# Kernel tuning notes

Measured on AMD Instinct MI355X. Metric: run time of the kernel, lower is better.

The kernel has to match this reference:

```python
import jax, jax.numpy as jnp
import numpy as np

N, F, E, A, H = 50000, 64, 1600000, 8, 16
RECEPTIVE_FIELD = 7


def setup_inputs() -> dict:
    key = jax.random.key(0)
    ks = jax.random.split(key, 12)
    inp = {
        "x": jax.random.normal(ks[0], (N, F), dtype=jnp.float32),
        "edge_index": jax.random.randint(ks[1], (2, E), 0, N, dtype=jnp.int64),
        "w1": jax.random.normal(ks[2], (F, H), dtype=jnp.float32) * 0.1,
        "b1": jax.random.normal(ks[3], (H,), dtype=jnp.float32) * 0.1,
        "w2": jax.random.normal(ks[4], (H, H), dtype=jnp.float32) * 0.1,
        "b2": jax.random.normal(ks[5], (H,), dtype=jnp.float32) * 0.1,
        "w3": jax.random.normal(ks[6], (H, F), dtype=jnp.float32) * 0.1,
        "b3": jax.random.normal(ks[7], (F,), dtype=jnp.float32) * 0.1,
        "fc1_w": jax.random.normal(ks[8], ((1 + RECEPTIVE_FIELD) * F, F), dtype=jnp.float32) * 0.05,
        "fc1_b": jax.random.normal(ks[9], (F,), dtype=jnp.float32) * 0.05,
        "fc2_w": jax.random.normal(ks[10], (F, A), dtype=jnp.float32) * 0.1,
        "fc2_b": jax.random.normal(ks[11], (A,), dtype=jnp.float32) * 0.1,
    }
    return inp


def _mlp(x, w1, b1, w2, b2, w3, b3):
    h = jax.nn.relu(x @ w1 + b1)
    h = jax.nn.relu(h @ w2 + b2)
    return h @ w3 + b3


def _agg_mean(x, src, dst):
    # scatter-mean: mean of source-node features over incoming edges per target
    s = jax.ops.segment_sum(x[src], dst, num_segments=N)          # [N, F]
    cnt = jax.ops.segment_sum(jnp.ones((src.shape[0], 1), x.dtype), dst, num_segments=N)
    return s / jnp.maximum(cnt, 1.0)  # nodes with no in-edges -> 0 (torch mean aggr)


def reference(x, edge_index, w1, b1, w2, b2, w3, b3, fc1_w, fc1_b, fc2_w, fc2_b):
    src, dst = edge_index[0], edge_index[1]
    mlp = lambda t: _mlp(t, w1, b1, w2, b2, w3, b3)
    fields = [mlp(mlp(x))]
    for i in range(RECEPTIVE_FIELD):
        x_ = mlp(x)
        for _ in range(i + 1):
            x_ = _agg_mean(x_, src, dst)
        fields.append(mlp(x_))
    f = jnp.concatenate(fields, axis=1)          # [N, 8*F]
    h = f @ fc1_w + fc1_b                        # [N, F]
    logits = h @ fc2_w + fc2_b                   # [N, A]
    return jax.nn.softmax(logits, axis=-1)       # Categorical probs
```

## Files before the change

### kernel.cpp

```cpp
#include <hip/hip_runtime.h>
#include <hip/hip_fp16.h>


#define NB2MAX 400
#define NBLK   256
#define CAP2   32
#define CAPC   48
#define CAPB   6144
#define OVCAP  1024
#define LCAP   6144
#define CAPN   64

__global__ __launch_bounds__(1024) void binfill_k(
    const int* __restrict__ src, const int* __restrict__ dst, int E, int n,
    int* __restrict__ gcur, int* __restrict__ ovbuf,
    int* __restrict__ bins, int* __restrict__ cnts,
    const float* __restrict__ w1, const float* __restrict__ w3,
    const float* __restrict__ b3, const float* __restrict__ fc1w,
    const float* __restrict__ fc1b, const float* __restrict__ fc2w,
    const float* __restrict__ fc2b,
    float* __restrict__ M, float* __restrict__ cvec,
    float* __restrict__ W31, float* __restrict__ c31) {
    __shared__ int lbuf[NB2MAX * CAP2];
    __shared__ int lcnt[NB2MAX];
    __shared__ int lflush[NB2MAX];
    int tid = threadIdx.x;
    int NB = (n + 127) >> 7;

    if ((int)blockIdx.x >= NBLK) {
        float* fl = (float*)lbuf;
        int s = (int)blockIdx.x - NBLK;
        if (s == 0) {
            if (tid < 256) {
                int i = tid >> 4, j = tid & 15;
                float a = 0.f;
                for (int g = 0; g < 64; g++) a += w3[i * 64 + g] * w1[g * 16 + j];
                W31[tid] = a;
            } else if (tid < 272) {
                int j = tid - 256;
                float a = 0.f;
                for (int g = 0; g < 64; g++) a += b3[g] * w1[g * 16 + j];
                c31[j] = a;
            } else if (tid >= 320 && tid < 384) {
                int h = tid - 320;
                float a = 0.f;
                for (int r = 0; r < 512; r++) a += b3[r & 63] * fc1w[r * 64 + h];
                fl[h] = a;
            }
            __syncthreads();
            if (tid < 8) {
                float a = fc2b[tid];
                for (int h = 0; h < 64; h++) a += (fc1b[h] + fl[h]) * fc2w[h * 8 + tid];
                cvec[tid] = a;
            }
        } else {
            int k = s - 1;
            {
                int i = tid >> 6, h = tid & 63;
                float a = 0.f;
                const float* f1 = fc1w + (size_t)(k * 64) * 64 + h;
                for (int g = 0; g < 64; g++) a += w3[i * 64 + g] * f1[g * 64];
                fl[i * 64 + h] = a;
            }
            __syncthreads();
            if (tid < 128) {
                int i = tid >> 3, j = tid & 7;
                float a = 0.f;
                for (int h = 0; h < 64; h++) a += fl[i * 64 + h] * fc2w[h * 8 + j];
                M[k * 128 + i * 8 + j] = a;
            }
        }
        return;
    }

    for (int b = tid; b < NB; b += 1024) { lcnt[b] = 0; lflush[b] = 0; }
    __syncthreads();
    int blk = blockIdx.x;
    int chunk = (E + NBLK - 1) / NBLK;
    int beg = blk * chunk;
    int end = beg + chunk; if (end > E) end = E;
    for (int t0 = beg; t0 < end; t0 += 1024) {
        int e = t0 + tid;
        if (e < end) {
            int d = dst[e], s = src[e];
            if ((unsigned)d < (unsigned)n && (unsigned)s < (unsigned)n) {
                int b = d >> 7;
                int pk = ((d & 127) << 16) | s;
                int pos = atomicAdd(&lcnt[b], 1);
                if (pos < CAP2) lbuf[b * CAP2 + pos] = pk;
                else {
                    int p = atomicAdd(&gcur[b], 1);
                    if (p < OVCAP) ovbuf[b * OVCAP + p] = pk;
                }
            }
        }
        __syncthreads();
        for (int b = tid; b < NB; b += 1024) {
            int cnt = lcnt[b]; if (cnt > CAP2) cnt = CAP2;
            int fl2 = lflush[b];
            size_t cell = ((size_t)b * NBLK + blk) * CAPC;
            int base = 0;
            while (cnt - base >= 16) {
                if (fl2 + 16 <= CAPC) {
                    int* dp = bins + cell + fl2;
                    #pragma unroll
                    for (int q = 0; q < 16; q++) dp[q] = lbuf[b * CAP2 + base + q];
                    fl2 += 16;
                } else {
                    int p = atomicAdd(&gcur[b], 16);
                    for (int q = 0; q < 16; q++)
                        if (p + q < OVCAP) ovbuf[b * OVCAP + p + q] = lbuf[b * CAP2 + base + q];
                }
                base += 16;
            }
            int rem = cnt - base;
            if (base > 0)
                for (int q = 0; q < rem; q++) lbuf[b * CAP2 + q] = lbuf[b * CAP2 + base + q];
            lcnt[b] = rem; lflush[b] = fl2;
        }
        __syncthreads();
    }
    for (int b = tid; b < NB; b += 1024) {
        int cnt = lcnt[b]; if (cnt > CAP2) cnt = CAP2;
        int fl2 = lflush[b];
        size_t cell = ((size_t)b * NBLK + blk) * CAPC;
        if (fl2 + cnt <= CAPC) {
            for (int q = 0; q < cnt; q++) bins[cell + fl2 + q] = lbuf[b * CAP2 + q];
            fl2 += cnt;
        } else {
            int p = atomicAdd(&gcur[b], cnt);
            for (int q = 0; q < cnt; q++)
                if (p + q < OVCAP) ovbuf[b * OVCAP + p + q] = lbuf[b * CAP2 + q];
        }
        cnts[(size_t)blk * NB + b] = fl2;
    }
}

struct SmemC {
    int hist[128], pref[128], cur[128], slot[128];
    int scnt[NBLK];
    int lbuf[LCAP];
    int sov;
    int ccnt[3], cbase[3];
};
struct SmemP {
    float sx[16 * 68];
    float sw1[1024], sw2[256], sW[256], sM[128];
    float sb1[16], sb2[16], sc[16], scv[8];
};
union SmemU { SmemC c; SmemP p; };

__global__ __launch_bounds__(256) void csr2proj_k(
    const int* __restrict__ bins, const int* __restrict__ cnts,
    const int* __restrict__ gcur, const int* __restrict__ ovbuf,
    unsigned short* __restrict__ csrp_s, int2* __restrict__ nd_s,
    int* __restrict__ csr, int2* __restrict__ be, int* __restrict__ lcnt3,
    const float* __restrict__ x, __half* __restrict__ z0, __half* __restrict__ z1,
    float* __restrict__ logits,
    const float* __restrict__ w1, const float* __restrict__ b1,
    const float* __restrict__ w2, const float* __restrict__ b2,
    const float* __restrict__ W31, const float* __restrict__ c31,
    const float* __restrict__ M0, const float* __restrict__ cvec,
    int n, int NBARG) {
    __shared__ SmemU smem;
    int tid = threadIdx.x;
    if ((int)blockIdx.x < NBARG) {
        SmemC& sc_ = smem.c;
        int NB = NBARG;
        int b = blockIdx.x;
        if (tid < 128) { sc_.hist[tid] = 0; sc_.cur[tid] = 0; }
        if (tid < 3) sc_.ccnt[tid] = 0;
        sc_.scnt[tid] = cnts[(size_t)tid * NB + b];
        if (tid == 0) {
            int g = gcur[b];
            sc_.sov = g < 0 ? 0 : (g > OVCAP ? OVCAP : g);
        }
        __syncthreads();
        {
            int c = sc_.scnt[tid];
            size_t cell = ((size_t)b * NBLK + tid) * CAPC;
            for (int i = 0; i < c; i++) atomicAdd(&sc_.hist[bins[cell + i] >> 16], 1);
        }
        if (tid == 0)
            for (int i = 0; i < sc_.sov; i++)
                atomicAdd(&sc_.hist[ovbuf[b * OVCAP + i] >> 16], 1);
        __syncthreads();
        if (tid == 0) {
            int r = 0;
            for (int i = 0; i < 128; i++) { sc_.pref[i] = r; r += sc_.hist[i]; }
        }
        __syncthreads();
        {
            int c = sc_.scnt[tid];
            size_t cell = ((size_t)b * NBLK + tid) * CAPC;
            for (int i = 0; i < c; i++) {
                int pk = bins[cell + i];
                int dl = pk >> 16;
                int pos = sc_.pref[dl] + atomicAdd(&sc_.cur[dl], 1);
                if (pos < LCAP) sc_.lbuf[pos] = pk & 0xffff;
            }
        }
        if (tid == 0) {
            for (int i = 0; i < sc_.sov; i++) {
                int pk = ovbuf[b * OVCAP + i];
                int dl = pk >> 16;
                int pos = sc_.pref[dl] + atomicAdd(&sc_.cur[dl], 1);
                if (pos < LCAP) sc_.lbuf[pos] = pk & 0xffff;
            }
        }
        __syncthreads();
        int myc = -1, lpos = 0;
        if (tid < 128) {
            int d = (b << 7) + tid;
            if (d < n) {
                int cnt = sc_.hist[tid];
                myc = cnt <= 32 ? 0 : (cnt <= 48 ? 1 : 2);
                lpos = atomicAdd(&sc_.ccnt[myc], 1);
            }
        }
        __syncthreads();
        if (tid < 3) sc_.cbase[tid] = atomicAdd(&lcnt3[tid], sc_.ccnt[tid]);
        __syncthreads();
        if (myc >= 0) {
            int d = (b << 7) + tid;
            int cnt = sc_.hist[tid];
            int s = myc * n + sc_.cbase[myc] + lpos;
            sc_.slot[tid] = s;
            nd_s[s] = make_int2(d, cnt);
            if (cnt > CAPN) {
                int s0 = b * CAPB + sc_.pref[tid];
                be[d] = make_int2(s0 + CAPN, s0 + cnt);
                for (int j = CAPN; j < cnt; j++)
                    csr[s0 + j] = sc_.lbuf[sc_.pref[tid] + j] << 2;
            }
        }
        __syncthreads();
        for (int q = tid; q < 128 * CAPN; q += 256) {
            int dl = q >> 6, j = q & 63;
            int d = (b << 7) + dl;
            if (d >= n) break;
            int cnt = sc_.hist[dl];
            int v = (j < cnt) ? sc_.lbuf[sc_.pref[dl] + j] : n;
            int pos = ((j & 3) << 4) | (j >> 2);
            csrp_s[(size_t)sc_.slot[dl] * CAPN + pos] = (unsigned short)v;
        }
        return;
    }
    SmemP& sp = smem.p;
    for (int i = tid; i < 1024; i += 256) sp.sw1[i] = w1[i];
    sp.sw2[tid] = w2[tid];
    sp.sW[tid] = W31[tid];
    if (tid < 128) sp.sM[tid] = M0[tid];
    if (tid < 16) { sp.sb1[tid] = b1[tid]; sp.sb2[tid] = b2[tid]; sp.sc[tid] = c31[tid]; }
    if (tid < 8) sp.scv[tid] = cvec[tid];
    if ((int)blockIdx.x == NBARG && tid < 16) {
        ((unsigned short*)z0)[(size_t)n * 16 + tid] = 0;
        ((unsigned short*)z1)[(size_t)n * 16 + tid] = 0;
    }
    int node0 = ((int)blockIdx.x - NBARG) * 16;
    {
        int r = tid >> 4, c4 = tid & 15;
        if (node0 + r < n) {
            float4 v = ((const float4*)(x + (size_t)(node0 + r) * 64))[c4];
            float* dstp = sp.sx + r * 68 + c4 * 4;
            dstp[0] = v.x; dstp[1] = v.y; dstp[2] = v.z; dstp[3] = v.w;
        }
    }
    __syncthreads();
    int nl = tid >> 4, jj = tid & 15;
    int node = node0 + nl;
    if (node >= n) return;
    float t1 = 0.f;
    const float* xr = sp.sx + nl * 68;
    #pragma unroll
    for (int g = 0; g < 64; g++) t1 += xr[g] * sp.sw1[g * 16 + jj];
    t1 = fmaxf(t1 + sp.sb1[jj], 0.f);
    float t2 = sp.sb2[jj];
    #pragma unroll
    for (int i = 0; i < 16; i++) t2 += __shfl(t1, i, 16) * sp.sw2[i * 16 + jj];
    t2 = fmaxf(t2, 0.f);
    float zv = sp.sc[jj];
    #pragma unroll
    for (int i = 0; i < 16; i++) zv += __shfl(t2, i, 16) * sp.sW[i * 16 + jj];
    z0[(size_t)node * 16 + jj] = __float2half(zv);
    float hv = fmaxf(zv + sp.sb1[jj], 0.f);
    float f2 = sp.sb2[jj];
    #pragma unroll
    for (int i = 0; i < 16; i++) f2 += __shfl(hv, i, 16) * sp.sw2[i * 16 + jj];
    f2 = fmaxf(f2, 0.f);
    float p0 = f2 * sp.sM[jj * 8 + 0], p1 = f2 * sp.sM[jj * 8 + 1];
    float p2 = f2 * sp.sM[jj * 8 + 2], p3 = f2 * sp.sM[jj * 8 + 3];
    float p4 = f2 * sp.sM[jj * 8 + 4], p5 = f2 * sp.sM[jj * 8 + 5];
    float p6 = f2 * sp.sM[jj * 8 + 6], p7 = f2 * sp.sM[jj * 8 + 7];
    #pragma unroll
    for (int off = 1; off < 16; off <<= 1) {
        p0 += __shfl_xor(p0, off, 16); p1 += __shfl_xor(p1, off, 16);
        p2 += __shfl_xor(p2, off, 16); p3 += __shfl_xor(p3, off, 16);
        p4 += __shfl_xor(p4, off, 16); p5 += __shfl_xor(p5, off, 16);
        p6 += __shfl_xor(p6, off, 16); p7 += __shfl_xor(p7, off, 16);
    }
    if (jj < 8) {
        float myp = jj == 0 ? p0 : jj == 1 ? p1 : jj == 2 ? p2 : jj == 3 ? p3
                  : jj == 4 ? p4 : jj == 5 ? p5 : jj == 6 ? p6 : p7;
        logits[(size_t)node * 8 + jj] = sp.scv[jj] + myp;
    }
}

__device__ __forceinline__ void acc_row(uint2 u, float& ax, float& ay,
                                        float& az, float& aw) {
    __half2 p = *reinterpret_cast<const __half2*>(&u.x);
    __half2 q = *reinterpret_cast<const __half2*>(&u.y);
    float2 f = __half22float2(p), g = __half22float2(q);
    ax += f.x; ay += f.y; az += g.x; aw += g.y;
}

__global__ __launch_bounds__(256, 4) void hop_k(
    const __half* __restrict__ zin, __half* __restrict__ zout,
    float* __restrict__ logits,
    const unsigned short* __restrict__ csrp_s, const int2* __restrict__ nd_s,
    const int2* __restrict__ be, const int* __restrict__ csr,
    const int* __restrict__ lcnt3,
    const float* __restrict__ w2, const float* __restrict__ b1,
    const float* __restrict__ b2, const float* __restrict__ M, int n, int FB) {
    __shared__ float sw2[256], sM[128], sb1[16], sb2[16];
    int tid = threadIdx.x;
    if ((int)blockIdx.x < FB) {
        sw2[tid] = w2[tid];
        if (tid < 128) sM[tid] = M[tid];
        if (tid < 16) { sb1[tid] = b1[tid]; sb2[tid] = b2[tid]; }
        __syncthreads();
        int nid = blockIdx.x * 256 + tid;
        if (nid >= n) return;
        float h[16];
        const __half2* zp = (const __half2*)(zin + (size_t)nid * 16);
        #pragma unroll
        for (int q = 0; q < 8; q++) {
            float2 f = __half22float2(zp[q]);
            h[2 * q] = f.x; h[2 * q + 1] = f.y;
        }
        #pragma unroll
        for (int i = 0; i < 16; i++) h[i] = fmaxf(h[i] + sb1[i], 0.f);
        float t2[16];
        #pragma unroll
        for (int j = 0; j < 16; j++) {
            float a = sb2[j];
            #pragma unroll
            for (int i = 0; i < 16; i++) a += h[i] * sw2[i * 16 + j];
            t2[j] = fmaxf(a, 0.f);
        }
        float* lp = logits + (size_t)nid * 8;
        #pragma unroll
        for (int j = 0; j < 8; j++) {
            float l = 0.f;
            #pragma unroll
            for (int i = 0; i < 16; i++) l += t2[i] * sM[i * 8 + j];
            lp[j] += l;
        }
        return;
    }
    int wave = tid >> 6;
    int lane = tid & 63;
    int quarter = lane >> 4;
    int l16 = lane & 15;
    int t4 = l16 >> 2, ch = l16 & 3;
    int idx = (((int)blockIdx.x - FB) * 4 + wave) * 4 + quarter;
    if (idx >= n) return;
    int ns = lcnt3[0], nm = lcnt3[1];
    int tier; size_t row;
    if (idx < ns)           { tier = 0; row = (size_t)idx; }
    else if (idx < ns + nm) { tier = 1; row = (size_t)n + (idx - ns); }
    else                    { tier = 2; row = 2 * (size_t)n + (idx - ns - nm); }
    int2 nd = nd_s[row];
    int node = nd.x, degi = nd.y;
    const uint4* ip = (const uint4*)(csrp_s + (row << 6));
    uint4 pa = ip[t4 * 2];
    int r0 = pa.x & 0xffff, r1 = pa.x >> 16;
    int r2 = pa.y & 0xffff, r3 = pa.y >> 16;
    int r4 = pa.z & 0xffff, r5 = pa.z >> 16;
    int r6 = pa.w & 0xffff, r7 = pa.w >> 16;
    const uint2* z2 = (const uint2*)zin;
    uint2 u0 = z2[((size_t)r0 << 2) + ch];
    uint2 u1 = z2[((size_t)r1 << 2) + ch];
    uint2 u2 = z2[((size_t)r2 << 2) + ch];
    uint2 u3 = z2[((size_t)r3 << 2) + ch];
    uint2 u4 = z2[((size_t)r4 << 2) + ch];
    uint2 u5 = z2[((size_t)r5 << 2) + ch];
    uint2 u6 = z2[((size_t)r6 << 2) + ch];
    uint2 u7 = z2[((size_t)r7 << 2) + ch];
    float ax = 0.f, ay = 0.f, az = 0.f, aw = 0.f;
    acc_row(u0, ax, ay, az, aw); acc_row(u1, ax, ay, az, aw);
    acc_row(u2, ax, ay, az, aw); acc_row(u3, ax, ay, az, aw);
    acc_row(u4, ax, ay, az, aw); acc_row(u5, ax, ay, az, aw);
    acc_row(u6, ax, ay, az, aw); acc_row(u7, ax, ay, az, aw);
    if (tier >= 1) {
        uint4 pb = ip[t4 * 2 + 1];
        int r8 = pb.x & 0xffff, r9 = pb.x >> 16;
        int rA = pb.y & 0xffff, rB = pb.y >> 16;
        uint2 u8 = z2[((size_t)r8 << 2) + ch];
        uint2 u9 = z2[((size_t)r9 << 2) + ch];
        uint2 uA = z2[((size_t)rA << 2) + ch];
        uint2 uB = z2[((size_t)rB << 2) + ch];
        acc_row(u8, ax, ay, az, aw); acc_row(u9, ax, ay, az, aw);
        acc_row(uA, ax, ay, az, aw); acc_row(uB, ax, ay, az, aw);
        if (tier == 2) {
            int rC = pb.z & 0xffff, rD = pb.z >> 16;
            int rE = pb.w & 0xffff, rF = pb.w >> 16;
            uint2 uC = z2[((size_t)rC << 2) + ch];
            uint2 uD = z2[((size_t)rD << 2) + ch];
            uint2 uE = z2[((size_t)rE << 2) + ch];
            uint2 uF = z2[((size_t)rF << 2) + ch];
            acc_row(uC, ax, ay, az, aw); acc_row(uD, ax, ay, az, aw);
            acc_row(uE, ax, ay, az, aw); acc_row(uF, ax, ay, az, aw);
            if (degi > CAPN) {
                int2 r = be[node];
                for (int q = r.x + t4; q < r.y; q += 4) {
                    uint2 u = z2[(size_t)csr[q] + ch];
                    acc_row(u, ax, ay, az, aw);
                }
            }
        }
    }
    #pragma unroll
    for (int off = 8; off >= 4; off >>= 1) {
        ax += __shfl_down(ax, off, 16);
        ay += __shfl_down(ay, off, 16);
        az += __shfl_down(az, off, 16);
        aw += __shfl_down(aw, off, 16);
    }
    if (l16 < 4) {
        float inv = 1.f / (float)(degi > 0 ? degi : 1);
        __half2 h01 = __floats2half2_rn(ax * inv, ay * inv);
        __half2 h23 = __floats2half2_rn(az * inv, aw * inv);
        uint2 w;
        w.x = *reinterpret_cast<unsigned int*>(&h01);
        w.y = *reinterpret_cast<unsigned int*>(&h23);
        ((uint2*)(zout + (size_t)node * 16))[l16] = w;
    }
}

__global__ __launch_bounds__(256, 4) void fieldsoft_k(
    const __half* __restrict__ z, float* __restrict__ logits,
    const float* __restrict__ w2, const float* __restrict__ b1,
    const float* __restrict__ b2, const float* __restrict__ M, int n) {
    __shared__ float sw2[256], sM[128], sb1[16], sb2[16];
    int tid = threadIdx.x;
    sw2[tid] = w2[tid];
    if (tid < 128) sM[tid] = M[tid];
    if (tid < 16) { sb1[tid] = b1[tid]; sb2[tid] = b2[tid]; }
    __syncthreads();
    int nl = tid >> 4, jj = tid & 15;
    int node = blockIdx.x * 16 + nl;
    if (node >= n) return;
    float zv = __half2float(z[(size_t)node * 16 + jj]);
    float hv = fmaxf(zv + sb1[jj], 0.f);
    float t2 = sb2[jj];
    #pragma unroll
    for (int i = 0; i < 16; i++) t2 += __shfl(hv, i, 16) * sw2[i * 16 + jj];
    t2 = fmaxf(t2, 0.f);
    float p0 = t2 * sM[jj * 8 + 0], p1 = t2 * sM[jj * 8 + 1];
    float p2 = t2 * sM[jj * 8 + 2], p3 = t2 * sM[jj * 8 + 3];
    float p4 = t2 * sM[jj * 8 + 4], p5 = t2 * sM[jj * 8 + 5];
    float p6 = t2 * sM[jj * 8 + 6], p7 = t2 * sM[jj * 8 + 7];
    #pragma unroll
    for (int off = 1; off < 16; off <<= 1) {
        p0 += __shfl_xor(p0, off, 16); p1 += __shfl_xor(p1, off, 16);
        p2 += __shfl_xor(p2, off, 16); p3 += __shfl_xor(p3, off, 16);
        p4 += __shfl_xor(p4, off, 16); p5 += __shfl_xor(p5, off, 16);
        p6 += __shfl_xor(p6, off, 16); p7 += __shfl_xor(p7, off, 16);
    }
    int q = jj & 7;
    float myp = q == 0 ? p0 : q == 1 ? p1 : q == 2 ? p2 : q == 3 ? p3
              : q == 4 ? p4 : q == 5 ? p5 : q == 6 ? p6 : p7;
    float lg = myp + logits[(size_t)node * 8 + q];
    float m = lg;
    m = fmaxf(m, __shfl_xor(m, 1, 8));
    m = fmaxf(m, __shfl_xor(m, 2, 8));
    m = fmaxf(m, __shfl_xor(m, 4, 8));
    float e = expf(lg - m);
    float s = e;
    s += __shfl_xor(s, 1, 8);
    s += __shfl_xor(s, 2, 8);
    s += __shfl_xor(s, 4, 8);
    if (jj < 8) logits[(size_t)node * 8 + jj] = e / s;
}

extern "C" void kernel_launch(void* const* d_in, const int* in_sizes, int n_in,
                              void* d_out, int out_size, void* d_ws, size_t ws_size,
                              hipStream_t stream) {
    const float* x    = (const float*)d_in[0];
    const int*   ei   = (const int*)d_in[1];
    const float* w1   = (const float*)d_in[2];
    const float* b1   = (const float*)d_in[3];
    const float* w2   = (const float*)d_in[4];
    const float* b2   = (const float*)d_in[5];
    const float* w3   = (const float*)d_in[6];
    const float* b3   = (const float*)d_in[7];
    const float* fc1w = (const float*)d_in[8];
    const float* fc1b = (const float*)d_in[9];
    const float* fc2w = (const float*)d_in[10];
    const float* fc2b = (const float*)d_in[11];
    float* out = (float*)d_out;

    int n = in_sizes[0] / 64;
    int E = in_sizes[1] / 2;
    int NB = (n + 127) >> 7;
    const int* src = ei;
    const int* dst = ei + E;

    char* ws = (char*)d_ws;
    auto carve = [&](size_t bytes) {
        char* p = ws;
        ws += (bytes + 255) & ~((size_t)255);
        return p;
    };
    int*   gcur    = (int*)carve((size_t)NB * 4);
    int*   lcnt3   = (int*)carve(16);
    int*   ovbuf   = (int*)carve((size_t)NB * OVCAP * 4);
    int*   binsbuf = (int*)carve((size_t)NB * NBLK * CAPC * 4);
    int*   cnts    = (int*)carve((size_t)NBLK * NB * 4);
    unsigned short* csrp_s = (unsigned short*)carve((size_t)3 * n * CAPN * 2);
    int2*  nd_s    = (int2*)carve((size_t)3 * n * 8);
    int*   csr     = (int*)carve((size_t)NB * CAPB * 4);
    int2*  be      = (int2*)carve((size_t)n * 8);
    __half* buf0   = (__half*)carve((size_t)(n + 1) * 16 * 2);
    __half* buf1   = (__half*)carve((size_t)(n + 1) * 16 * 2);
    float* M       = (float*)carve(1024 * 4);
    float* cvec    = (float*)carve(8 * 4);
    float* W31     = (float*)carve(256 * 4);
    float* c31     = (float*)carve(16 * 4);

    size_t gpad = ((size_t)NB * 4 + 255) & ~((size_t)255);
    hipMemsetAsync(gcur, 0, gpad + 16, stream);
    binfill_k<<<NBLK + 9, 1024, 0, stream>>>(src, dst, E, n, gcur, ovbuf, binsbuf, cnts,
                                             w1, w3, b3, fc1w, fc1b, fc2w, fc2b,
                                             M, cvec, W31, c31);

    int FB  = (n + 255) / 256;
    int FBJ = (n + 15) / 16;
    int AB  = (n + 15) / 16;
    csr2proj_k<<<NB + FBJ, 256, 0, stream>>>(binsbuf, cnts, gcur, ovbuf,
                                             csrp_s, nd_s, csr, be, lcnt3,
                                             x, buf0, buf1, out, w1, b1, w2, b2,
                                             W31, c31, M, cvec, n, NB);

    __half* cur = buf0;
    __half* nxt = buf1;
    hop_k<<<AB, 256, 0, stream>>>(cur, nxt, out, csrp_s, nd_s, be, csr, lcnt3,
                                  w2, b1, b2, M, n, 0);
    { __half* t = cur; cur = nxt; nxt = t; }
    for (int k = 1; k <= 6; k++) {
        hop_k<<<FB + AB, 256, 0, stream>>>(cur, nxt, out, csrp_s, nd_s, be, csr,
                                           lcnt3, w2, b1, b2, M + k * 128, n, FB);
        __half* t = cur; cur = nxt; nxt = t;
    }
    fieldsoft_k<<<FBJ, 256, 0, stream>>>(cur, out, w2, b1, b2, M + 7 * 128, n);
}
```

Baseline: 235.6 us.

## Assign one wave per node in hop gather and drop degree-tier sorting

Replaces the degree-tiered slot layout (a quarter-wave per node, with nodes bucketed by degree through global atomics) with a plain per-node padded CSR and a full 64-lane wave per node. Each lane group loads two or four neighbours and reduces across the wave with xor shuffles. Occupancy hint raised to 6. This removes the tier bookkeeping and the indirection through the slot table, but assigns four times as many lanes per node, so low-degree nodes leave many lanes idle.

```diff
diff --git a/kernel.cpp b/kernel.cpp
--- a/kernel.cpp
+++ b/kernel.cpp
@@ -137,11 +137,10 @@
 }
 
 struct SmemC {
-    int hist[128], pref[128], cur[128], slot[128];
+    int hist[128], pref[128], cur[128];
     int scnt[NBLK];
     int lbuf[LCAP];
     int sov;
-    int ccnt[3], cbase[3];
 };
 struct SmemP {
     float sx[16 * 68];
@@ -153,8 +152,8 @@
 __global__ __launch_bounds__(256) void csr2proj_k(
     const int* __restrict__ bins, const int* __restrict__ cnts,
     const int* __restrict__ gcur, const int* __restrict__ ovbuf,
-    unsigned short* __restrict__ csrp_s, int2* __restrict__ nd_s,
-    int* __restrict__ csr, int2* __restrict__ be, int* __restrict__ lcnt3,
+    unsigned short* __restrict__ csrp, int* __restrict__ degs,
+    int* __restrict__ csr, int2* __restrict__ be,
     const float* __restrict__ x, __half* __restrict__ z0, __half* __restrict__ z1,
     float* __restrict__ logits,
     const float* __restrict__ w1, const float* __restrict__ b1,
@@ -169,7 +168,6 @@
         int NB = NBARG;
         int b = blockIdx.x;
         if (tid < 128) { sc_.hist[tid] = 0; sc_.cur[tid] = 0; }
-        if (tid < 3) sc_.ccnt[tid] = 0;
         sc_.scnt[tid] = cnts[(size_t)tid * NB + b];
         if (tid == 0) {
             int g = gcur[b];
@@ -209,29 +207,17 @@
             }
         }
         __syncthreads();
-        int myc = -1, lpos = 0;
         if (tid < 128) {
             int d = (b << 7) + tid;
             if (d < n) {
                 int cnt = sc_.hist[tid];
-                myc = cnt <= 32 ? 0 : (cnt <= 48 ? 1 : 2);
-                lpos = atomicAdd(&sc_.ccnt[myc], 1);
-            }
-        }
-        __syncthreads();
-        if (tid < 3) sc_.cbase[tid] = atomicAdd(&lcnt3[tid], sc_.ccnt[tid]);
-        __syncthreads();
-        if (myc >= 0) {
-            int d = (b << 7) + tid;
-            int cnt = sc_.hist[tid];
-            int s = myc * n + sc_.cbase[myc] + lpos;
-            sc_.slot[tid] = s;
-            nd_s[s] = make_int2(d, cnt);
-            if (cnt > CAPN) {
-                int s0 = b * CAPB + sc_.pref[tid];
-                be[d] = make_int2(s0 + CAPN, s0 + cnt);
-                for (int j = CAPN; j < cnt; j++)
-                    csr[s0 + j] = sc_.lbuf[sc_.pref[tid] + j] << 2;
+                degs[d] = cnt;
+                if (cnt > CAPN) {
+                    int s0 = b * CAPB + sc_.pref[tid];
+                    be[d] = make_int2(s0 + CAPN, s0 + cnt);
+                    for (int j = CAPN; j < cnt; j++)
+                        csr[s0 + j] = sc_.lbuf[sc_.pref[tid] + j] << 2;
+                }
             }
         }
         __syncthreads();
@@ -241,8 +227,8 @@
             if (d >= n) break;
             int cnt = sc_.hist[dl];
             int v = (j < cnt) ? sc_.lbuf[sc_.pref[dl] + j] : n;
-            int pos = ((j & 3) << 4) | (j >> 2);
-            csrp_s[(size_t)sc_.slot[dl] * CAPN + pos] = (unsigned short)v;
+            int pos = ((j & 15) << 2) | (j >> 4);
+            csrp[(size_t)d * CAPN + pos] = (unsigned short)v;
         }
         return;
     }
@@ -314,12 +300,11 @@
     ax += f.x; ay += f.y; az += g.x; aw += g.y;
 }
 
-__global__ __launch_bounds__(256, 4) void hop_k(
+__global__ __launch_bounds__(256, 6) void hop_k(
     const __half* __restrict__ zin, __half* __restrict__ zout,
     float* __restrict__ logits,
-    const unsigned short* __restrict__ csrp_s, const int2* __restrict__ nd_s,
+    const unsigned short* __restrict__ csrp, const int* __restrict__ degs,
     const int2* __restrict__ be, const int* __restrict__ csr,
-    const int* __restrict__ lcnt3,
     const float* __restrict__ w2, const float* __restrict__ b1,
     const float* __restrict__ b2, const float* __restrict__ M, int n, int FB) {
     __shared__ float sw2[256], sM[128], sb1[16], sb2[16];
@@ -360,81 +345,49 @@
     }
     int wave = tid >> 6;
     int lane = tid & 63;
-    int quarter = lane >> 4;
-    int l16 = lane & 15;
-    int t4 = l16 >> 2, ch = l16 & 3;
-    int idx = (((int)blockIdx.x - FB) * 4 + wave) * 4 + quarter;
-    if (idx >= n) return;
-    int ns = lcnt3[0], nm = lcnt3[1];
-    int tier; size_t row;
-    if (idx < ns)           { tier = 0; row = (size_t)idx; }
-    else if (idx < ns + nm) { tier = 1; row = (size_t)n + (idx - ns); }
-    else                    { tier = 2; row = 2 * (size_t)n + (idx - ns - nm); }
-    int2 nd = nd_s[row];
-    int node = nd.x, degi = nd.y;
-    const uint4* ip = (const uint4*)(csrp_s + (row << 6));
-    uint4 pa = ip[t4 * 2];
-    int r0 = pa.x & 0xffff, r1 = pa.x >> 16;
-    int r2 = pa.y & 0xffff, r3 = pa.y >> 16;
-    int r4 = pa.z & 0xffff, r5 = pa.z >> 16;
-    int r6 = pa.w & 0xffff, r7 = pa.w >> 16;
+    int sg = lane >> 2, ch = lane & 3;
+    int node = ((int)blockIdx.x - FB) * 4 + wave;
+    if (node >= n) return;
+    int degi = degs[node];
+    const unsigned int* ip = (const unsigned int*)(csrp + ((size_t)node << 6));
+    unsigned int pa = ip[sg * 2];
+    int r0 = pa & 0xffff, r1 = pa >> 16;
     const uint2* z2 = (const uint2*)zin;
     uint2 u0 = z2[((size_t)r0 << 2) + ch];
     uint2 u1 = z2[((size_t)r1 << 2) + ch];
-    uint2 u2 = z2[((size_t)r2 << 2) + ch];
-    uint2 u3 = z2[((size_t)r3 << 2) + ch];
-    uint2 u4 = z2[((size_t)r4 << 2) + ch];
-    uint2 u5 = z2[((size_t)r5 << 2) + ch];
-    uint2 u6 = z2[((size_t)r6 << 2) + ch];
-    uint2 u7 = z2[((size_t)r7 << 2) + ch];
     float ax = 0.f, ay = 0.f, az = 0.f, aw = 0.f;
-    acc_row(u0, ax, ay, az, aw); acc_row(u1, ax, ay, az, aw);
-    acc_row(u2, ax, ay, az, aw); acc_row(u3, ax, ay, az, aw);
-    acc_row(u4, ax, ay, az, aw); acc_row(u5, ax, ay, az, aw);
-    acc_row(u6, ax, ay, az, aw); acc_row(u7, ax, ay, az, aw);
-    if (tier >= 1) {
-        uint4 pb = ip[t4 * 2 + 1];
-        int r8 = pb.x & 0xffff, r9 = pb.x >> 16;
-        int rA = pb.y & 0xffff, rB = pb.y >> 16;
-        uint2 u8 = z2[((size_t)r8 << 2) + ch];
-        uint2 u9 = z2[((size_t)r9 << 2) + ch];
-        uint2 uA = z2[((size_t)rA << 2) + ch];
-        uint2 uB = z2[((size_t)rB << 2) + ch];
-        acc_row(u8, ax, ay, az, aw); acc_row(u9, ax, ay, az, aw);
-        acc_row(uA, ax, ay, az, aw); acc_row(uB, ax, ay, az, aw);
-        if (tier == 2) {
-            int rC = pb.z & 0xffff, rD = pb.z >> 16;
-            int rE = pb.w & 0xffff, rF = pb.w >> 16;
-            uint2 uC = z2[((size_t)rC << 2) + ch];
-            uint2 uD = z2[((size_t)rD << 2) + ch];
-            uint2 uE = z2[((size_t)rE << 2) + ch];
-            uint2 uF = z2[((size_t)rF << 2) + ch];
-            acc_row(uC, ax, ay, az, aw); acc_row(uD, ax, ay, az, aw);
-            acc_row(uE, ax, ay, az, aw); acc_row(uF, ax, ay, az, aw);
-            if (degi > CAPN) {
-                int2 r = be[node];
-                for (int q = r.x + t4; q < r.y; q += 4) {
-                    uint2 u = z2[(size_t)csr[q] + ch];
-                    acc_row(u, ax, ay, az, aw);
-                }
-            }
-        }
-    }
-    #pragma unroll
-    for (int off = 8; off >= 4; off >>= 1) {
-        ax += __shfl_down(ax, off, 16);
-        ay += __shfl_down(ay, off, 16);
-        az += __shfl_down(az, off, 16);
-        aw += __shfl_down(aw, off, 16);
-    }
-    if (l16 < 4) {
+    acc_row(u0, ax, ay, az, aw);
+    acc_row(u1, ax, ay, az, aw);
+    if (degi > 32) {
+        unsigned int pb = ip[sg * 2 + 1];
+        int r2 = pb & 0xffff, r3 = pb >> 16;
+        uint2 u2 = z2[((size_t)r2 << 2) + ch];
+        uint2 u3 = z2[((size_t)r3 << 2) + ch];
+        acc_row(u2, ax, ay, az, aw);
+        acc_row(u3, ax, ay, az, aw);
+        if (degi > CAPN) {
+            int2 r = be[node];
+            for (int q = r.x + sg; q < r.y; q += 16) {
+                uint2 u = z2[(size_t)csr[q] + ch];
+                acc_row(u, ax, ay, az, aw);
+            }
+        }
+    }
+    #pragma unroll
+    for (int off = 4; off <= 32; off <<= 1) {
+        ax += __shfl_xor(ax, off, 64);
+        ay += __shfl_xor(ay, off, 64);
+        az += __shfl_xor(az, off, 64);
+        aw += __shfl_xor(aw, off, 64);
+    }
+    if (lane < 4) {
         float inv = 1.f / (float)(degi > 0 ? degi : 1);
         __half2 h01 = __floats2half2_rn(ax * inv, ay * inv);
         __half2 h23 = __floats2half2_rn(az * inv, aw * inv);
         uint2 w;
         w.x = *reinterpret_cast<unsigned int*>(&h01);
         w.y = *reinterpret_cast<unsigned int*>(&h23);
-        ((uint2*)(zout + (size_t)node * 16))[l16] = w;
+        ((uint2*)(zout + (size_t)node * 16))[lane] = w;
     }
 }
 
@@ -514,12 +467,11 @@
         return p;
     };
     int*   gcur    = (int*)carve((size_t)NB * 4);
-    int*   lcnt3   = (int*)carve(16);
     int*   ovbuf   = (int*)carve((size_t)NB * OVCAP * 4);
     int*   binsbuf = (int*)carve((size_t)NB * NBLK * CAPC * 4);
     int*   cnts    = (int*)carve((size_t)NBLK * NB * 4);
-    unsigned short* csrp_s = (unsigned short*)carve((size_t)3 * n * CAPN * 2);
-    int2*  nd_s    = (int2*)carve((size_t)3 * n * 8);
+    unsigned short* csrp = (unsigned short*)carve((size_t)n * CAPN * 2);
+    int*   degs    = (int*)carve((size_t)n * 4);
     int*   csr     = (int*)carve((size_t)NB * CAPB * 4);
     int2*  be      = (int2*)carve((size_t)n * 8);
     __half* buf0   = (__half*)carve((size_t)(n + 1) * 16 * 2);
@@ -529,28 +481,27 @@
     float* W31     = (float*)carve(256 * 4);
     float* c31     = (float*)carve(16 * 4);
 
-    size_t gpad = ((size_t)NB * 4 + 255) & ~((size_t)255);
-    hipMemsetAsync(gcur, 0, gpad + 16, stream);
+    hipMemsetAsync(gcur, 0, (size_t)NB * 4, stream);
     binfill_k<<<NBLK + 9, 1024, 0, stream>>>(src, dst, E, n, gcur, ovbuf, binsbuf, cnts,
                                              w1, w3, b3, fc1w, fc1b, fc2w, fc2b,
                                              M, cvec, W31, c31);
 
     int FB  = (n + 255) / 256;
     int FBJ = (n + 15) / 16;
-    int AB  = (n + 15) / 16;
+    int AB  = (n + 3) / 4;
     csr2proj_k<<<NB + FBJ, 256, 0, stream>>>(binsbuf, cnts, gcur, ovbuf,
-                                             csrp_s, nd_s, csr, be, lcnt3,
+                                             csrp, degs, csr, be,
                                              x, buf0, buf1, out, w1, b1, w2, b2,
                                              W31, c31, M, cvec, n, NB);
 
     __half* cur = buf0;
     __half* nxt = buf1;
-    hop_k<<<AB, 256, 0, stream>>>(cur, nxt, out, csrp_s, nd_s, be, csr, lcnt3,
+    hop_k<<<AB, 256, 0, stream>>>(cur, nxt, out, csrp, degs, be, csr,
                                   w2, b1, b2, M, n, 0);
     { __half* t = cur; cur = nxt; nxt = t; }
     for (int k = 1; k <= 6; k++) {
-        hop_k<<<FB + AB, 256, 0, stream>>>(cur, nxt, out, csrp_s, nd_s, be, csr,
-                                           lcnt3, w2, b1, b2, M + k * 128, n, FB);
+        hop_k<<<FB + AB, 256, 0, stream>>>(cur, nxt, out, csrp, degs, be, csr,
+                                           w2, b1, b2, M + k * 128, n, FB);
         __half* t = cur; cur = nxt; nxt = t;
     }
     fieldsoft_k<<<FBJ, 256, 0, stream>>>(cur, out, w2, b1, b2, M + 7 * 128, n);
```

New measurement: 274.7 us. +16.6%, slower.
